# Kernel optimization log

Measured on AMD Instinct MI355X. Metric: run time of the kernel, lower is better.

The kernel has to match this reference:

```python
import jax, jax.numpy as jnp
import numpy as np

B, H, L, T, D = 2, 12, 1024, 1024, 64
FEA = 3
DIM = H * D  # 768


def setup_inputs() -> dict:
    key = jax.random.key(0)
    ks = jax.random.split(key, 8)
    return {
        "s0": jax.random.normal(ks[0], (B, H, L, T), jnp.float32),
        "s1": jax.random.normal(ks[1], (B, H, L, T), jnp.float32),
        "s2": jax.random.normal(ks[2], (B, H, L, T), jnp.float32),
        "v": jax.random.normal(ks[3], (B, H, T, D), jnp.float32),
        "fuse_w": jax.random.normal(ks[4], (H, H * FEA), jnp.float32) * 0.1,
        "fuse_b": jax.random.normal(ks[5], (H,), jnp.float32) * 0.1,
        "proj_w": jax.random.normal(ks[6], (DIM, DIM), jnp.float32) * 0.02,
        "proj_b": jax.random.normal(ks[7], (DIM,), jnp.float32) * 0.02,
    }


def reference(s0, s1, s2, v, fuse_w, fuse_b, proj_w, proj_b):
    # concat score maps along channel dim: [b, h*fea, l, t]
    scores = jnp.concatenate([s0, s1, s2], axis=1)
    # 1x1 conv fusion over channel dim: [b, h, l, t]
    fused = jnp.einsum('bclt,oc->bolt', scores, fuse_w) + fuse_b[None, :, None, None]
    # softmax over keys (last dim)
    attn = jax.nn.softmax(fused, axis=-1)
    # attn @ V: [b, h, l, d]
    x = jnp.einsum('bhlt,bhtd->bhld', attn, v)
    # merge heads: [b, l, h*d]
    b, h, l, d = x.shape
    x = jnp.transpose(x, (0, 2, 1, 3)).reshape(b, l, h * d)
    # output projection (torch Linear: x @ W.T + b)
    return x @ proj_w.T + proj_b
```

## Files before the change

### kernel.cpp

```cpp
#include <hip/hip_runtime.h>
#include <hip/hip_bf16.h>

typedef __attribute__((ext_vector_type(8))) short short8;
typedef __attribute__((ext_vector_type(8))) unsigned short ushort8;
typedef __attribute__((ext_vector_type(4))) unsigned short u16x4;
typedef __attribute__((ext_vector_type(4))) float f32x4;

#define NB 2
#define NH 12
#define NL 1024
#define NT 1024
#define ND 64
#define NCH 36
#define DIM 768

static __device__ __forceinline__ unsigned short f2bf(float x) {
  union { float f; unsigned int u; } c; c.f = x;
  unsigned int r = c.u + 0x7fffu + ((c.u >> 16) & 1u);
  return (unsigned short)(r >> 16);
}

static __device__ __forceinline__ void gload_lds16(const float* g, float* l) {
  __builtin_amdgcn_global_load_lds(
      (const __attribute__((address_space(1))) void*)g,
      (__attribute__((address_space(3))) void*)l, 16, 0, 0);
}

__global__ __launch_bounds__(1024) void k_fuse_softmax(
    const float* __restrict__ s0, const float* __restrict__ s1,
    const float* __restrict__ s2, const float* __restrict__ wT,
    unsigned short* __restrict__ attn)
{
  __shared__ float buf[2][2][4][NT];
  const int tid = threadIdx.x;
  const int wv = tid >> 6, lane = tid & 63;
  const int r = wv >> 2, q = wv & 3;
  const int b = blockIdx.x >> 8;
  const int l = ((blockIdx.x & 255) << 2) | r;
  const int toff = q * 256 + lane * 4;

  float acc[NH][4];
#pragma unroll
  for (int h = 0; h < NH; ++h) {
    acc[h][0] = 0.f; acc[h][1] = 0.f; acc[h][2] = 0.f; acc[h][3] = 0.f;
  }

  const size_t rowbase = (size_t)b * NH * NL * NT + (size_t)l * NT + toff;
  const float* pall[3] = { s0 + rowbase, s1 + rowbase, s2 + rowbase };

#define K1_SRC(c) (pall[(c) / 12] + (size_t)((c) % 12) * NL * NT)

  gload_lds16(K1_SRC(0), &buf[0][0][r][toff]);
  gload_lds16(K1_SRC(1), &buf[0][1][r][toff]);

#pragma unroll
  for (int bt = 0; bt < 18; ++bt) {
    if (bt < 17) {
      gload_lds16(K1_SRC(2 * bt + 2), &buf[(bt + 1) & 1][0][r][toff]);
      gload_lds16(K1_SRC(2 * bt + 3), &buf[(bt + 1) & 1][1][r][toff]);
      asm volatile("s_waitcnt vmcnt(2)" ::: "memory");
    } else {
      asm volatile("s_waitcnt vmcnt(0)" ::: "memory");
    }
    __builtin_amdgcn_sched_barrier(0);
#pragma unroll
    for (int j = 0; j < 2; ++j) {
      const int c = 2 * bt + j;
      const float4 sv = *(const float4*)&buf[bt & 1][j][r][toff];
      const float* wp = wT + c * NH;
#pragma unroll
      for (int h = 0; h < NH; ++h) {
        const float w = wp[h];
        acc[h][0] = fmaf(w, sv.x, acc[h][0]);
        acc[h][1] = fmaf(w, sv.y, acc[h][1]);
        acc[h][2] = fmaf(w, sv.z, acc[h][2]);
        acc[h][3] = fmaf(w, sv.w, acc[h][3]);
      }
    }
  }
#undef K1_SRC

  __syncthreads();
  float* red = &buf[0][0][0][0];

  float mx[NH];
#pragma unroll
  for (int h = 0; h < NH; ++h) {
    mx[h] = fmaxf(fmaxf(acc[h][0], acc[h][1]), fmaxf(acc[h][2], acc[h][3]));
#pragma unroll
    for (int off = 32; off > 0; off >>= 1)
      mx[h] = fmaxf(mx[h], __shfl_xor(mx[h], off));
  }
  if (lane == 0) {
#pragma unroll
    for (int h = 0; h < NH; ++h) red[wv * NH + h] = mx[h];
  }
  __syncthreads();
#pragma unroll
  for (int h = 0; h < NH; ++h)
    mx[h] = fmaxf(fmaxf(red[(r * 4 + 0) * NH + h], red[(r * 4 + 1) * NH + h]),
                  fmaxf(red[(r * 4 + 2) * NH + h], red[(r * 4 + 3) * NH + h]));

  float sm[NH];
#pragma unroll
  for (int h = 0; h < NH; ++h) {
    acc[h][0] = __expf(acc[h][0] - mx[h]);
    acc[h][1] = __expf(acc[h][1] - mx[h]);
    acc[h][2] = __expf(acc[h][2] - mx[h]);
    acc[h][3] = __expf(acc[h][3] - mx[h]);
    sm[h] = (acc[h][0] + acc[h][1]) + (acc[h][2] + acc[h][3]);
#pragma unroll
    for (int off = 32; off > 0; off >>= 1)
      sm[h] += __shfl_xor(sm[h], off);
  }
  if (lane == 0) {
#pragma unroll
    for (int h = 0; h < NH; ++h) red[192 + wv * NH + h] = sm[h];
  }
  __syncthreads();

#pragma unroll
  for (int h = 0; h < NH; ++h) {
    float s = (red[192 + (r * 4 + 0) * NH + h] + red[192 + (r * 4 + 1) * NH + h]) +
              (red[192 + (r * 4 + 2) * NH + h] + red[192 + (r * 4 + 3) * NH + h]);
    float inv = 1.0f / s;
    u16x4 u;
    u[0] = f2bf(acc[h][0] * inv);
    u[1] = f2bf(acc[h][1] * inv);
    u[2] = f2bf(acc[h][2] * inv);
    u[3] = f2bf(acc[h][3] * inv);
    *(u16x4*)(attn + ((size_t)(b * NH + h) * NL + l) * NT + toff) = u;
  }
}

__global__ __launch_bounds__(256) void k_transpose_v(
    const float* __restrict__ v, const float* __restrict__ fw,
    unsigned short* __restrict__ vT, float* __restrict__ wT)
{
  __shared__ float vS[128][65];
  const int tid = threadIdx.x;
  const int tt = blockIdx.x;
  const int h = blockIdx.y, b = blockIdx.z;
  if (tt == 0 && h == 0 && b == 0) {
    for (int i = tid; i < NCH * NH; i += 256) {
      int c = i / NH, hh = i % NH;
      wT[c * NH + hh] = fw[hh * NCH + c];
    }
  }
  const int t0 = tt * 128;
  const float* vp = v + ((size_t)(b * NH + h) * NT + t0) * ND;
#pragma unroll
  for (int r = 0; r < 8; ++r) {
    int f = tid + r * 256;
    int t = f >> 4, d4 = (f & 15) * 4;
    float4 x = *(const float4*)(vp + (size_t)t * ND + d4);
    vS[t][d4 + 0] = x.x; vS[t][d4 + 1] = x.y;
    vS[t][d4 + 2] = x.z; vS[t][d4 + 3] = x.w;
  }
  __syncthreads();
  unsigned short* op = vT + (size_t)(b * NH + h) * ND * NT;
#pragma unroll
  for (int r = 0; r < 4; ++r) {
    int c = tid + r * 256;
    int d = c >> 4, tl = (c & 15) * 8;
    ushort8 u;
#pragma unroll
    for (int j = 0; j < 8; ++j) u[j] = f2bf(vS[tl + j][d]);
    *(ushort8*)(op + (size_t)d * NT + t0 + tl) = u;
  }
}

__global__ __launch_bounds__(128) void k_pv(
    const unsigned short* __restrict__ attn,
    const unsigned short* __restrict__ vT,
    unsigned short* __restrict__ xb)
{
  __shared__ unsigned short vS[64][136];
  const int tid = threadIdx.x;
  const int lane = tid & 63, wv = tid >> 6;
  const int lt = blockIdx.x, h = blockIdx.y, b = blockIdx.z;
  const int l0 = lt * 32;
  const unsigned short* ap = attn + ((size_t)(b * NH + h) * NL + l0) * NT;
  const unsigned short* vp = vT + (size_t)(b * NH + h) * ND * NT;
  f32x4 acc[4] = {};
  const int arow = wv * 16 + (lane & 15);
  const int kg = (lane >> 4) * 8;
  const int bn = lane & 15;

  for (int kt = 0; kt < 8; ++kt) {
    __syncthreads();
#pragma unroll
    for (int r = 0; r < 8; ++r) {
      int c = tid + r * 128;
      int d = c >> 4, tl = (c & 15) * 8;
      *(ushort8*)&vS[d][tl] = *(const ushort8*)(vp + (size_t)d * NT + kt * 128 + tl);
    }
    __syncthreads();
#pragma unroll
    for (int ks = 0; ks < 4; ++ks) {
      short8 af = *(const short8*)(ap + (size_t)arow * NT + kt * 128 + ks * 32 + kg);
#pragma unroll
      for (int dt = 0; dt < 4; ++dt) {
        short8 bf = *(const short8*)&vS[dt * 16 + bn][ks * 32 + kg];
        acc[dt] = __builtin_amdgcn_mfma_f32_16x16x32_bf16(af, bf, acc[dt], 0, 0, 0);
      }
    }
  }
  const int crow0 = wv * 16 + (lane >> 4) * 4;
#pragma unroll
  for (int dt = 0; dt < 4; ++dt) {
#pragma unroll
    for (int r = 0; r < 4; ++r) {
      int row = l0 + crow0 + r;
      xb[((size_t)b * NL + row) * DIM + h * ND + dt * 16 + bn] = f2bf(acc[dt][r]);
    }
  }
}

__global__ __launch_bounds__(256) void k_proj(
    const unsigned short* __restrict__ xb, const float* __restrict__ pw,
    const float* __restrict__ pb, float* __restrict__ out)
{
  __shared__ unsigned short wS[64][136];
  const int tid = threadIdx.x;
  const int lane = tid & 63, wv = tid >> 6;
  const int n0 = blockIdx.x * 64, o0 = blockIdx.y * 64;
  f32x4 acc[4] = {};
  const int kg = (lane >> 4) * 8;
  const int bn = lane & 15;
  const int arow = n0 + wv * 16 + bn;

  for (int kt = 0; kt < 6; ++kt) {
    __syncthreads();
#pragma unroll
    for (int r = 0; r < 4; ++r) {
      int c = tid + r * 256;
      int oi = c >> 4, kl = (c & 15) * 8;
      const float* wp = pw + (size_t)(o0 + oi) * DIM + kt * 128 + kl;
      float4 x0 = *(const float4*)(wp);
      float4 x1 = *(const float4*)(wp + 4);
      ushort8 u;
      u[0] = f2bf(x0.x); u[1] = f2bf(x0.y); u[2] = f2bf(x0.z); u[3] = f2bf(x0.w);
      u[4] = f2bf(x1.x); u[5] = f2bf(x1.y); u[6] = f2bf(x1.z); u[7] = f2bf(x1.w);
      *(ushort8*)&wS[oi][kl] = u;
    }
    __syncthreads();
#pragma unroll
    for (int ks = 0; ks < 4; ++ks) {
      short8 af = *(const short8*)(xb + (size_t)arow * DIM + kt * 128 + ks * 32 + kg);
#pragma unroll
      for (int ot = 0; ot < 4; ++ot) {
        short8 bf = *(const short8*)&wS[ot * 16 + bn][ks * 32 + kg];
        acc[ot] = __builtin_amdgcn_mfma_f32_16x16x32_bf16(af, bf, acc[ot], 0, 0, 0);
      }
    }
  }
  const int crow0 = wv * 16 + (lane >> 4) * 4;
#pragma unroll
  for (int ot = 0; ot < 4; ++ot) {
    const int oc = o0 + ot * 16 + bn;
    const float bias = pb[oc];
#pragma unroll
    for (int r = 0; r < 4; ++r) {
      int row = n0 + crow0 + r;
      out[(size_t)row * DIM + oc] = acc[ot][r] + bias;
    }
  }
}

extern "C" void kernel_launch(void* const* d_in, const int* in_sizes, int n_in,
                              void* d_out, int out_size, void* d_ws, size_t ws_size,
                              hipStream_t stream) {
  const float* s0 = (const float*)d_in[0];
  const float* s1 = (const float*)d_in[1];
  const float* s2 = (const float*)d_in[2];
  const float* v  = (const float*)d_in[3];
  const float* fw = (const float*)d_in[4];
  const float* pw = (const float*)d_in[6];
  const float* pb = (const float*)d_in[7];
  float* out = (float*)d_out;

  const size_t attn_bytes = (size_t)NB * NH * NL * NT * 2;
  const size_t vT_bytes   = (size_t)NB * NH * ND * NT * 2;
  const size_t xb_bytes   = (size_t)NB * NL * DIM * 2;
  unsigned short* attn = (unsigned short*)d_ws;
  unsigned short* vT   = (unsigned short*)((char*)d_ws + attn_bytes);
  unsigned short* xb   = (unsigned short*)((char*)d_ws + attn_bytes + vT_bytes);
  float*          wT   = (float*)((char*)d_ws + attn_bytes + vT_bytes + xb_bytes);

  k_transpose_v<<<dim3(8, NH, NB), dim3(256), 0, stream>>>(v, fw, vT, wT);
  k_fuse_softmax<<<dim3(NB * 256), dim3(1024), 0, stream>>>(s0, s1, s2, wT, attn);
  k_pv<<<dim3(32, NH, NB), dim3(128), 0, stream>>>(attn, vT, xb);
  k_proj<<<dim3(32, DIM / 64), dim3(256), 0, stream>>>(xb, pw, pb, out);
}
```

Measured before the change: 121.7 us.

## Use one-row 256-thread blocks with a 4-stage LDS prefetch pipeline in fuse-softmax

The fuse-softmax kernel now processes one query row per 256-thread block instead of four rows per 1024-thread block, launching 2048 blocks. The LDS staging buffer goes from double to quadruple buffering, with three channel-pairs issued ahead and vmcnt waits adjusted to match. The aim is to keep more global loads in flight and get finer-grained scheduling and occupancy on this memory-bound kernel. In exchange, each block runs more barrier and reduction steps per row and carries a deeper buffer.

```diff
diff --git a/kernel.cpp b/kernel.cpp
--- a/kernel.cpp
+++ b/kernel.cpp
@@ -26,18 +26,17 @@
       (__attribute__((address_space(3))) void*)l, 16, 0, 0);
 }
 
-__global__ __launch_bounds__(1024) void k_fuse_softmax(
+__global__ __launch_bounds__(256) void k_fuse_softmax(
     const float* __restrict__ s0, const float* __restrict__ s1,
     const float* __restrict__ s2, const float* __restrict__ wT,
     unsigned short* __restrict__ attn)
 {
-  __shared__ float buf[2][2][4][NT];
+  __shared__ float buf[4][2][NT];
   const int tid = threadIdx.x;
+  const int b = blockIdx.x >> 10;
+  const int l = blockIdx.x & 1023;
   const int wv = tid >> 6, lane = tid & 63;
-  const int r = wv >> 2, q = wv & 3;
-  const int b = blockIdx.x >> 8;
-  const int l = ((blockIdx.x & 255) << 2) | r;
-  const int toff = q * 256 + lane * 4;
+  const int t4 = tid * 4;
 
   float acc[NH][4];
 #pragma unroll
@@ -45,19 +44,25 @@
     acc[h][0] = 0.f; acc[h][1] = 0.f; acc[h][2] = 0.f; acc[h][3] = 0.f;
   }
 
-  const size_t rowbase = (size_t)b * NH * NL * NT + (size_t)l * NT + toff;
-  const float* pall[3] = { s0 + rowbase, s1 + rowbase, s2 + rowbase };
+  const size_t base = (size_t)b * NH * NL * NT + (size_t)l * NT + t4;
+  const float* pall[3] = { s0 + base, s1 + base, s2 + base };
 
 #define K1_SRC(c) (pall[(c) / 12] + (size_t)((c) % 12) * NL * NT)
-
-  gload_lds16(K1_SRC(0), &buf[0][0][r][toff]);
-  gload_lds16(K1_SRC(1), &buf[0][1][r][toff]);
+#define K1_ISSUE(BT) do {                                                     \
+    gload_lds16(K1_SRC(2 * (BT)),     &buf[(BT) & 3][0][t4]);                 \
+    gload_lds16(K1_SRC(2 * (BT) + 1), &buf[(BT) & 3][1][t4]);                 \
+  } while (0)
+
+  K1_ISSUE(0); K1_ISSUE(1); K1_ISSUE(2);
 
 #pragma unroll
   for (int bt = 0; bt < 18; ++bt) {
-    if (bt < 17) {
-      gload_lds16(K1_SRC(2 * bt + 2), &buf[(bt + 1) & 1][0][r][toff]);
-      gload_lds16(K1_SRC(2 * bt + 3), &buf[(bt + 1) & 1][1][r][toff]);
+    if (bt < 15) {
+      K1_ISSUE(bt + 3);
+      asm volatile("s_waitcnt vmcnt(6)" ::: "memory");
+    } else if (bt == 15) {
+      asm volatile("s_waitcnt vmcnt(4)" ::: "memory");
+    } else if (bt == 16) {
       asm volatile("s_waitcnt vmcnt(2)" ::: "memory");
     } else {
       asm volatile("s_waitcnt vmcnt(0)" ::: "memory");
@@ -66,7 +71,7 @@
 #pragma unroll
     for (int j = 0; j < 2; ++j) {
       const int c = 2 * bt + j;
-      const float4 sv = *(const float4*)&buf[bt & 1][j][r][toff];
+      const float4 sv = *(const float4*)&buf[bt & 3][j][t4];
       const float* wp = wT + c * NH;
 #pragma unroll
       for (int h = 0; h < NH; ++h) {
@@ -78,10 +83,11 @@
       }
     }
   }
+#undef K1_ISSUE
 #undef K1_SRC
 
   __syncthreads();
-  float* red = &buf[0][0][0][0];
+  float* red = &buf[0][0][0];
 
   float mx[NH];
 #pragma unroll
@@ -98,8 +104,8 @@
   __syncthreads();
 #pragma unroll
   for (int h = 0; h < NH; ++h)
-    mx[h] = fmaxf(fmaxf(red[(r * 4 + 0) * NH + h], red[(r * 4 + 1) * NH + h]),
-                  fmaxf(red[(r * 4 + 2) * NH + h], red[(r * 4 + 3) * NH + h]));
+    mx[h] = fmaxf(fmaxf(red[0 * NH + h], red[1 * NH + h]),
+                  fmaxf(red[2 * NH + h], red[3 * NH + h]));
 
   float sm[NH];
 #pragma unroll
@@ -115,21 +121,21 @@
   }
   if (lane == 0) {
 #pragma unroll
-    for (int h = 0; h < NH; ++h) red[192 + wv * NH + h] = sm[h];
+    for (int h = 0; h < NH; ++h) red[48 + wv * NH + h] = sm[h];
   }
   __syncthreads();
 
 #pragma unroll
   for (int h = 0; h < NH; ++h) {
-    float s = (red[192 + (r * 4 + 0) * NH + h] + red[192 + (r * 4 + 1) * NH + h]) +
-              (red[192 + (r * 4 + 2) * NH + h] + red[192 + (r * 4 + 3) * NH + h]);
+    float s = (red[48 + 0 * NH + h] + red[48 + 1 * NH + h]) +
+              (red[48 + 2 * NH + h] + red[48 + 3 * NH + h]);
     float inv = 1.0f / s;
     u16x4 u;
     u[0] = f2bf(acc[h][0] * inv);
     u[1] = f2bf(acc[h][1] * inv);
     u[2] = f2bf(acc[h][2] * inv);
     u[3] = f2bf(acc[h][3] * inv);
-    *(u16x4*)(attn + ((size_t)(b * NH + h) * NL + l) * NT + toff) = u;
+    *(u16x4*)(attn + ((size_t)(b * NH + h) * NL + l) * NT + t4) = u;
   }
 }
 
@@ -289,7 +295,7 @@
   float*          wT   = (float*)((char*)d_ws + attn_bytes + vT_bytes + xb_bytes);
 
   k_transpose_v<<<dim3(8, NH, NB), dim3(256), 0, stream>>>(v, fw, vT, wT);
-  k_fuse_softmax<<<dim3(NB * 256), dim3(1024), 0, stream>>>(s0, s1, s2, wT, attn);
+  k_fuse_softmax<<<dim3(NB * NL), dim3(256), 0, stream>>>(s0, s1, s2, wT, attn);
   k_pv<<<dim3(32, NH, NB), dim3(128), 0, stream>>>(attn, vT, xb);
   k_proj<<<dim3(32, DIM / 64), dim3(256), 0, stream>>>(xb, pw, pb, out);
 }
```

Result: no change. 123.1 us (+1.1%).
